# Kernel optimization log

Hardware: AMD Instinct MI355X
Metric: run time of the kernel (lower is better)

The kernel has to match this reference:

```python
import jax, jax.numpy as jnp
import numpy as np

IN_F = 4096
OUT_F = 4096
BLOCK = 8
N_CENTROIDS = 2048
N_BLOCKS = IN_F // BLOCK  # 512
N_TOKENS = 1024


def setup_inputs() -> dict:
    key = jax.random.key(0)
    k1, k2, k3, k4 = jax.random.split(key, 4)
    x = jax.random.normal(k1, (N_TOKENS, IN_F), dtype=jnp.float32)
    centroids = jax.random.normal(k2, (N_CENTROIDS, BLOCK), dtype=jnp.float32)
    # assignments: block-major layout, length n_blocks * out_features
    assignments = jax.random.randint(k3, (N_BLOCKS * OUT_F,), 0, N_CENTROIDS, dtype=jnp.int32)
    bias = jax.random.normal(k4, (OUT_F,), dtype=jnp.float32) * 0.01
    # counts = bincount(assignments), used only in backward (grad averaging)
    counts = jax.ops.segment_sum(
        jnp.ones_like(assignments, dtype=jnp.float32), assignments,
        num_segments=N_CENTROIDS)
    return {"x": x, "centroids": centroids, "bias": bias,
            "assignments": assignments, "counts": counts}


def reference(x, centroids, bias, assignments, counts):
    # weight = centroids[assignments].reshape(n_blocks, out_f, block)
    #                        .permute(1,0,2).reshape(out_f, in_f)
    w = centroids[assignments]  # [n_blocks*out_f, block]
    w = w.reshape(N_BLOCKS, OUT_F, BLOCK).transpose(1, 0, 2).reshape(OUT_F, IN_F)
    # F.linear(x, weight, bias) = x @ w.T + bias
    return x @ w.T + bias
```

## Files before the change

kernel.cpp:

```cpp
#include <hip/hip_runtime.h>
#include <hip/hip_bf16.h>

#define IN_F   4096
#define OUT_F  4096
#define QBLK   8
#define NBLKS  512
#define NTOK   1024
#define NCENT  2048

typedef unsigned int u32;
typedef unsigned short u16;
typedef __attribute__((ext_vector_type(8))) short short8;
typedef __attribute__((ext_vector_type(4))) float floatx4;

__device__ __forceinline__ u16 f2bf(float f) {
  union { float f; u32 u; } v; v.f = f;
  u32 u = v.u;
  return (u16)((u + 0x7fffu + ((u >> 16) & 1u)) >> 16);
}

__device__ __forceinline__ void load_lds_16(const void* g, void* l) {
  __builtin_amdgcn_global_load_lds(
      (const __attribute__((address_space(1))) u32*)g,
      (__attribute__((address_space(3))) u32*)l, 16, 0, 0);
}

__global__ __launch_bounds__(256) void cast_bf16_kernel(
    const float* __restrict__ src, u16* __restrict__ dst) {
  int g = blockIdx.x * 256 + threadIdx.x;
  const float4* sv = (const float4*)src;
  float4 a = sv[(size_t)g * 2];
  float4 b = sv[(size_t)g * 2 + 1];
  union { u16 s[8]; uint4 v; } o;
  o.s[0] = f2bf(a.x); o.s[1] = f2bf(a.y); o.s[2] = f2bf(a.z); o.s[3] = f2bf(a.w);
  o.s[4] = f2bf(b.x); o.s[5] = f2bf(b.y); o.s[6] = f2bf(b.z); o.s[7] = f2bf(b.w);
  ((uint4*)dst)[g] = o.v;
}

__global__ __launch_bounds__(256, 4) void gemm_fused_kernel(
    const u16* __restrict__ A,
    const u16* __restrict__ centb,
    const int* __restrict__ assign,
    const float* __restrict__ bias,
    float* __restrict__ out0,
    float* __restrict__ partials) {
  __shared__ __align__(16) u16 cs[NCENT * 8];
  __shared__ __align__(16) u16 As[128 * 32];

  const int t = threadIdx.x;
  const int lane = t & 63;
  const int wv = t >> 6;
  const int wm = wv >> 1;
  const int wn = wv & 1;
  const int quad = lane >> 4;
  const int r16 = lane & 15;
  const int m0 = blockIdx.y * 128;
  const int n0 = blockIdx.x * 128;
  const int s = blockIdx.z;
  const int kchunk = IN_F / gridDim.z;
  const int k_base = s * kchunk;
  const int iters = kchunk / 32;

#pragma unroll
  for (int it = 0; it < 8; ++it) {
    int c = it * 256 + t;
    load_lds_16(centb + (size_t)c * 8, cs + (size_t)c * 8);
  }

  floatx4 acc[4][4];
#pragma unroll
  for (int i = 0; i < 4; ++i)
#pragma unroll
    for (int j = 0; j < 4; ++j)
#pragma unroll
      for (int r = 0; r < 4; ++r) acc[i][j][r] = 0.0f;

  const int ncol = n0 + wn * 64 + r16;
  const int sq = quad ^ (r16 & 3);

  for (int kt = 0; kt < iters; ++kt) {
    const int k0 = k_base + kt * 32;

    int idxv[4];
    const int kb = (k0 >> 3) + quad;
#pragma unroll
    for (int j = 0; j < 4; ++j)
      idxv[j] = assign[(size_t)kb * OUT_F + ncol + j * 16];

#pragma unroll
    for (int i = 0; i < 2; ++i) {
      int p = i * 256 + t;
      int row = p >> 2;
      int q = (p & 3) ^ (row & 3);
      load_lds_16(A + (size_t)(m0 + row) * IN_F + k0 + q * 8, As + p * 8);
    }
    __syncthreads();

    const short8* Asv = (const short8*)As;
    const short8* csv = (const short8*)cs;
    short8 af[4], bfr[4];
#pragma unroll
    for (int i = 0; i < 4; ++i)
      af[i] = Asv[(wm * 64 + i * 16 + r16) * 4 + sq];
#pragma unroll
    for (int j = 0; j < 4; ++j)
      bfr[j] = csv[idxv[j]];

#pragma unroll
    for (int i = 0; i < 4; ++i)
#pragma unroll
      for (int j = 0; j < 4; ++j)
        acc[i][j] = __builtin_amdgcn_mfma_f32_16x16x32_bf16(af[i], bfr[j], acc[i][j], 0, 0, 0);

    __syncthreads();
  }

  float* C = (s == 0) ? out0 : (partials + (size_t)(s - 1) * NTOK * OUT_F);
  const bool add_bias = (gridDim.z == 1);
  const int row_base = m0 + wm * 64 + quad * 4;
#pragma unroll
  for (int j = 0; j < 4; ++j) {
    const int col = ncol + j * 16;
    const float bv = add_bias ? bias[col] : 0.0f;
#pragma unroll
    for (int i = 0; i < 4; ++i) {
      const int row = row_base + i * 16;
#pragma unroll
      for (int r = 0; r < 4; ++r)
        C[(size_t)(row + r) * OUT_F + col] = acc[i][j][r] + bv;
    }
  }
}

__global__ __launch_bounds__(256) void reduce_kernel(
    float* __restrict__ out, const float* __restrict__ partials,
    const float* __restrict__ bias, int sm1) {
  int g = blockIdx.x * 256 + threadIdx.x;
  float4 v = ((const float4*)out)[g];
  for (int s = 0; s < sm1; ++s) {
    float4 p = ((const float4*)(partials + (size_t)s * NTOK * OUT_F))[g];
    v.x += p.x; v.y += p.y; v.z += p.z; v.w += p.w;
  }
  float4 b = ((const float4*)bias)[g & (OUT_F / 4 - 1)];
  v.x += b.x; v.y += b.y; v.z += b.z; v.w += b.w;
  ((float4*)out)[g] = v;
}

extern "C" void kernel_launch(void* const* d_in, const int* in_sizes, int n_in,
                              void* d_out, int out_size, void* d_ws, size_t ws_size,
                              hipStream_t stream) {
  const float* x      = (const float*)d_in[0];
  const float* cent   = (const float*)d_in[1];
  const float* bias   = (const float*)d_in[2];
  const int*   assign = (const int*)d_in[3];
  float* out = (float*)d_out;

  const size_t xb_bytes   = (size_t)NTOK * IN_F * sizeof(u16);
  const size_t cent_bytes = (size_t)NCENT * 8 * sizeof(u16);
  const size_t part_bytes = (size_t)NTOK * OUT_F * sizeof(float);
  u16*   xb       = (u16*)d_ws;
  u16*   centb    = (u16*)((char*)d_ws + xb_bytes);
  float* partials = (float*)((char*)d_ws + xb_bytes + cent_bytes);

  const size_t base = xb_bytes + cent_bytes;
  int S = 1;
  if (ws_size >= base + 3 * part_bytes) S = 4;
  else if (ws_size >= base + 1 * part_bytes) S = 2;

  hipLaunchKernelGGL(cast_bf16_kernel, dim3((NTOK * IN_F / 8) / 256), dim3(256), 0, stream,
                     x, xb);
  hipLaunchKernelGGL(cast_bf16_kernel, dim3((NCENT * 8 / 8) / 256), dim3(256), 0, stream,
                     cent, centb);
  hipLaunchKernelGGL(gemm_fused_kernel, dim3(OUT_F / 128, NTOK / 128, S), dim3(256), 0, stream,
                     xb, centb, assign, bias, out, partials);
  if (S > 1)
    hipLaunchKernelGGL(reduce_kernel, dim3((NTOK * OUT_F / 4) / 256), dim3(256), 0, stream,
                       out, partials, bias, S - 1);
}
```

Baseline: 131.2 us.

## Pre-swizzle activations into fragment layout and register-prefetch A directly from global

The cast kernel now writes x in bf16 in a layout grouped by 16 rows and 8-element k-blocks, so each MFMA lane can load its A fragment straight from global memory with one 16-byte load. The A tile in LDS and both per-iteration barriers are removed, and the A fragments and assignment indices for the next k-step are prefetched into registers. MFMA issue priority is raised with setprio, and launch bounds drop to 3 waves per SIMD to make room for the extra registers. In exchange, A is no longer shared through LDS across the two N-waves of a block, so global and L2 traffic for activations roughly doubles.

```diff
diff --git a/kernel.cpp b/kernel.cpp
--- a/kernel.cpp
+++ b/kernel.cpp
@@ -37,15 +37,40 @@
   ((uint4*)dst)[g] = o.v;
 }
 
-__global__ __launch_bounds__(256, 4) void gemm_fused_kernel(
-    const u16* __restrict__ A,
+__global__ __launch_bounds__(256) void cast_swz_kernel(
+    const float* __restrict__ src, u16* __restrict__ dst) {
+  __shared__ __align__(16) u16 ls[256 * 8];
+  const int b = blockIdx.x;
+  const int mg = b >> 5;
+  const int kq = b & 31;
+  const int t = threadIdx.x;
+  const int ml = t >> 4;
+  const int kbl = t & 15;
+
+  const float* p = src + (size_t)(mg * 16 + ml) * IN_F + kq * 128 + kbl * 8;
+  float4 a = ((const float4*)p)[0];
+  float4 c = ((const float4*)p)[1];
+  union { u16 s[8]; uint4 v; } o;
+  o.s[0] = f2bf(a.x); o.s[1] = f2bf(a.y); o.s[2] = f2bf(a.z); o.s[3] = f2bf(a.w);
+  o.s[4] = f2bf(c.x); o.s[5] = f2bf(c.y); o.s[6] = f2bf(c.z); o.s[7] = f2bf(c.w);
+
+  const int cidx = (kbl << 4) | (ml ^ kbl);
+  *(uint4*)&ls[cidx * 8] = o.v;
+  __syncthreads();
+
+  const int g = (t & 0xF0) | ((t & 15) ^ ((t >> 4) & 15));
+  uint4* dbase = (uint4*)(dst + (size_t)(mg * 512 + kq * 16) * 128);
+  dbase[g] = ((const uint4*)ls)[t];
+}
+
+__global__ __launch_bounds__(256, 3) void gemm_fused_kernel(
+    const u16* __restrict__ xs,
     const u16* __restrict__ centb,
     const int* __restrict__ assign,
     const float* __restrict__ bias,
     float* __restrict__ out0,
     float* __restrict__ partials) {
   __shared__ __align__(16) u16 cs[NCENT * 8];
-  __shared__ __align__(16) u16 As[128 * 32];
 
   const int t = threadIdx.x;
   const int lane = t & 63;
@@ -58,7 +83,7 @@
   const int n0 = blockIdx.x * 128;
   const int s = blockIdx.z;
   const int kchunk = IN_F / gridDim.z;
-  const int k_base = s * kchunk;
+  const int kb0 = (s * kchunk) >> 3;
   const int iters = kchunk / 32;
 
 #pragma unroll
@@ -76,43 +101,52 @@
       for (int r = 0; r < 4; ++r) acc[i][j][r] = 0.0f;
 
   const int ncol = n0 + wn * 64 + r16;
-  const int sq = quad ^ (r16 & 3);
+  const short8* xv = (const short8*)xs;
+  const short8* csv = (const short8*)cs;
+
+  const int mgrp0 = (m0 >> 4) + wm * 4;
+  size_t abase[4];
+#pragma unroll
+  for (int i = 0; i < 4; ++i)
+    abase[i] = ((size_t)(mgrp0 + i) * 512 + kb0 + quad) * 16 + r16;
+
+  const int* aptr = assign + (size_t)(kb0 + quad) * OUT_F + ncol;
+
+  short8 afc[4];
+#pragma unroll
+  for (int i = 0; i < 4; ++i) afc[i] = xv[abase[i]];
+  int idxc[4];
+#pragma unroll
+  for (int j = 0; j < 4; ++j) idxc[j] = aptr[j * 16];
+
+  __syncthreads();
 
   for (int kt = 0; kt < iters; ++kt) {
-    const int k0 = k_base + kt * 32;
-
-    int idxv[4];
-    const int kb = (k0 >> 3) + quad;
-#pragma unroll
-    for (int j = 0; j < 4; ++j)
-      idxv[j] = assign[(size_t)kb * OUT_F + ncol + j * 16];
-
-#pragma unroll
-    for (int i = 0; i < 2; ++i) {
-      int p = i * 256 + t;
-      int row = p >> 2;
-      int q = (p & 3) ^ (row & 3);
-      load_lds_16(A + (size_t)(m0 + row) * IN_F + k0 + q * 8, As + p * 8);
+    short8 afn[4];
+    int idxn[4];
+    if (kt + 1 < iters) {
+#pragma unroll
+      for (int i = 0; i < 4; ++i) afn[i] = xv[abase[i] + (size_t)(kt + 1) * 64];
+#pragma unroll
+      for (int j = 0; j < 4; ++j) idxn[j] = aptr[(size_t)(kt + 1) * 4 * OUT_F + j * 16];
     }
-    __syncthreads();
-
-    const short8* Asv = (const short8*)As;
-    const short8* csv = (const short8*)cs;
-    short8 af[4], bfr[4];
+
+    short8 bfr[4];
+#pragma unroll
+    for (int j = 0; j < 4; ++j) bfr[j] = csv[idxc[j]];
+
+    __builtin_amdgcn_s_setprio(1);
 #pragma unroll
     for (int i = 0; i < 4; ++i)
-      af[i] = Asv[(wm * 64 + i * 16 + r16) * 4 + sq];
-#pragma unroll
-    for (int j = 0; j < 4; ++j)
-      bfr[j] = csv[idxv[j]];
-
-#pragma unroll
-    for (int i = 0; i < 4; ++i)
 #pragma unroll
       for (int j = 0; j < 4; ++j)
-        acc[i][j] = __builtin_amdgcn_mfma_f32_16x16x32_bf16(af[i], bfr[j], acc[i][j], 0, 0, 0);
-
-    __syncthreads();
+        acc[i][j] = __builtin_amdgcn_mfma_f32_16x16x32_bf16(afc[i], bfr[j], acc[i][j], 0, 0, 0);
+    __builtin_amdgcn_s_setprio(0);
+
+#pragma unroll
+    for (int i = 0; i < 4; ++i) afc[i] = afn[i];
+#pragma unroll
+    for (int j = 0; j < 4; ++j) idxc[j] = idxn[j];
   }
 
   float* C = (s == 0) ? out0 : (partials + (size_t)(s - 1) * NTOK * OUT_F);
@@ -158,7 +192,7 @@
   const size_t xb_bytes   = (size_t)NTOK * IN_F * sizeof(u16);
   const size_t cent_bytes = (size_t)NCENT * 8 * sizeof(u16);
   const size_t part_bytes = (size_t)NTOK * OUT_F * sizeof(float);
-  u16*   xb       = (u16*)d_ws;
+  u16*   xs       = (u16*)d_ws;
   u16*   centb    = (u16*)((char*)d_ws + xb_bytes);
   float* partials = (float*)((char*)d_ws + xb_bytes + cent_bytes);
 
@@ -167,12 +201,11 @@
   if (ws_size >= base + 3 * part_bytes) S = 4;
   else if (ws_size >= base + 1 * part_bytes) S = 2;
 
-  hipLaunchKernelGGL(cast_bf16_kernel, dim3((NTOK * IN_F / 8) / 256), dim3(256), 0, stream,
-                     x, xb);
+  hipLaunchKernelGGL(cast_swz_kernel, dim3(64 * 32), dim3(256), 0, stream, x, xs);
   hipLaunchKernelGGL(cast_bf16_kernel, dim3((NCENT * 8 / 8) / 256), dim3(256), 0, stream,
                      cent, centb);
   hipLaunchKernelGGL(gemm_fused_kernel, dim3(OUT_F / 128, NTOK / 128, S), dim3(256), 0, stream,
-                     xb, centb, assign, bias, out, partials);
+                     xs, centb, assign, bias, out, partials);
   if (S > 1)
     hipLaunchKernelGGL(reduce_kernel, dim3((NTOK * OUT_F / 4) / 256), dim3(256), 0, stream,
                        out, partials, bias, S - 1);
```

Result: slower. 136.7 us (+4.2%).

## Double-buffer A tile in LDS and prefetch next assignment indices

Applied to the files above, without the earlier changes.

Adds a second LDS buffer for the A tile and issues the next tile's global-to-LDS loads and next assignment-index loads before computing the current tile. The two per-iteration __syncthreads are replaced by one explicit vmcnt wait plus barrier, so global-load latency overlaps MFMA work. Split-K is now fixed at compile time to 4 and always uses the reduce kernel, no longer checking workspace size. That risks out-of-bounds writes if the workspace cannot hold three partial buffers, and the extra LDS buffer may lower occupancy.

```diff
diff --git a/kernel.cpp b/kernel.cpp
--- a/kernel.cpp
+++ b/kernel.cpp
@@ -7,6 +7,10 @@
 #define NBLKS  512
 #define NTOK   1024
 #define NCENT  2048
+
+#define SPLITK 4
+#define KCHUNK (IN_F / SPLITK)
+#define KITERS (KCHUNK / 32)
 
 typedef unsigned int u32;
 typedef unsigned short u16;
@@ -45,7 +49,7 @@
     float* __restrict__ out0,
     float* __restrict__ partials) {
   __shared__ __align__(16) u16 cs[NCENT * 8];
-  __shared__ __align__(16) u16 As[128 * 32];
+  __shared__ __align__(16) u16 As[2][128 * 32];
 
   const int t = threadIdx.x;
   const int lane = t & 63;
@@ -57,9 +61,8 @@
   const int m0 = blockIdx.y * 128;
   const int n0 = blockIdx.x * 128;
   const int s = blockIdx.z;
-  const int kchunk = IN_F / gridDim.z;
-  const int k_base = s * kchunk;
-  const int iters = kchunk / 32;
+  const int kb0 = (s * KCHUNK) >> 3;
+  const int k_base = kb0 << 3;
 
 #pragma unroll
   for (int it = 0; it < 8; ++it) {
@@ -67,6 +70,17 @@
     load_lds_16(centb + (size_t)c * 8, cs + (size_t)c * 8);
   }
 
+  {
+    const int p0 = t;
+#pragma unroll
+    for (int i = 0; i < 2; ++i) {
+      int p = i * 256 + p0;
+      int row = p >> 2;
+      int q = (p & 3) ^ (row & 3);
+      load_lds_16(A + (size_t)(m0 + row) * IN_F + k_base + q * 8, &As[0][p * 8]);
+    }
+  }
+
   floatx4 acc[4][4];
 #pragma unroll
   for (int i = 0; i < 4; ++i)
@@ -77,34 +91,42 @@
 
   const int ncol = n0 + wn * 64 + r16;
   const int sq = quad ^ (r16 & 3);
-
-  for (int kt = 0; kt < iters; ++kt) {
-    const int k0 = k_base + kt * 32;
-
-    int idxv[4];
-    const int kb = (k0 >> 3) + quad;
-#pragma unroll
-    for (int j = 0; j < 4; ++j)
-      idxv[j] = assign[(size_t)kb * OUT_F + ncol + j * 16];
-
-#pragma unroll
-    for (int i = 0; i < 2; ++i) {
-      int p = i * 256 + t;
-      int row = p >> 2;
-      int q = (p & 3) ^ (row & 3);
-      load_lds_16(A + (size_t)(m0 + row) * IN_F + k0 + q * 8, As + p * 8);
-    }
-    __syncthreads();
-
-    const short8* Asv = (const short8*)As;
-    const short8* csv = (const short8*)cs;
+  const int* ai = assign + (size_t)kb0 * OUT_F;
+  const u32 vi = (u32)(quad * OUT_F + ncol);
+
+  int idxc[4], idxn[4];
+#pragma unroll
+  for (int j = 0; j < 4; ++j) idxc[j] = ai[vi + (u32)(j * 16)];
+  __syncthreads();
+
+  const short8* csv = (const short8*)cs;
+  int buf = 0;
+
+  for (int kt = 0; kt < KITERS; ++kt) {
+    const bool not_last = (kt + 1 < KITERS);
+    if (not_last) {
+      const int k0n = k_base + (kt + 1) * 32;
+#pragma unroll
+      for (int i = 0; i < 2; ++i) {
+        int p = i * 256 + t;
+        int row = p >> 2;
+        int q = (p & 3) ^ (row & 3);
+        load_lds_16(A + (size_t)(m0 + row) * IN_F + k0n + q * 8,
+                    &As[buf ^ 1][p * 8]);
+      }
+      __builtin_amdgcn_sched_barrier(0);
+      const int* an = ai + (size_t)(kt + 1) * 4 * OUT_F;
+#pragma unroll
+      for (int j = 0; j < 4; ++j) idxn[j] = an[vi + (u32)(j * 16)];
+    }
+
+    const short8* Asv = (const short8*)As[buf];
     short8 af[4], bfr[4];
 #pragma unroll
     for (int i = 0; i < 4; ++i)
       af[i] = Asv[(wm * 64 + i * 16 + r16) * 4 + sq];
 #pragma unroll
-    for (int j = 0; j < 4; ++j)
-      bfr[j] = csv[idxv[j]];
+    for (int j = 0; j < 4; ++j) bfr[j] = csv[idxc[j]];
 
 #pragma unroll
     for (int i = 0; i < 4; ++i)
@@ -112,16 +134,25 @@
       for (int j = 0; j < 4; ++j)
         acc[i][j] = __builtin_amdgcn_mfma_f32_16x16x32_bf16(af[i], bfr[j], acc[i][j], 0, 0, 0);
 
-    __syncthreads();
+#pragma unroll
+    for (int j = 0; j < 4; ++j) idxc[j] = idxn[j];
+
+    if (not_last) {
+      __builtin_amdgcn_sched_barrier(0);
+      asm volatile("s_waitcnt vmcnt(4)" ::: "memory");
+      __builtin_amdgcn_sched_barrier(0);
+      __builtin_amdgcn_s_barrier();
+      __builtin_amdgcn_sched_barrier(0);
+    }
+    buf ^= 1;
   }
 
   float* C = (s == 0) ? out0 : (partials + (size_t)(s - 1) * NTOK * OUT_F);
-  const bool add_bias = (gridDim.z == 1);
   const int row_base = m0 + wm * 64 + quad * 4;
 #pragma unroll
   for (int j = 0; j < 4; ++j) {
     const int col = ncol + j * 16;
-    const float bv = add_bias ? bias[col] : 0.0f;
+    const float bv = 0.0f;
 #pragma unroll
     for (int i = 0; i < 4; ++i) {
       const int row = row_base + i * 16;
@@ -157,23 +188,16 @@
 
   const size_t xb_bytes   = (size_t)NTOK * IN_F * sizeof(u16);
   const size_t cent_bytes = (size_t)NCENT * 8 * sizeof(u16);
-  const size_t part_bytes = (size_t)NTOK * OUT_F * sizeof(float);
   u16*   xb       = (u16*)d_ws;
   u16*   centb    = (u16*)((char*)d_ws + xb_bytes);
   float* partials = (float*)((char*)d_ws + xb_bytes + cent_bytes);
-
-  const size_t base = xb_bytes + cent_bytes;
-  int S = 1;
-  if (ws_size >= base + 3 * part_bytes) S = 4;
-  else if (ws_size >= base + 1 * part_bytes) S = 2;
 
   hipLaunchKernelGGL(cast_bf16_kernel, dim3((NTOK * IN_F / 8) / 256), dim3(256), 0, stream,
                      x, xb);
   hipLaunchKernelGGL(cast_bf16_kernel, dim3((NCENT * 8 / 8) / 256), dim3(256), 0, stream,
                      cent, centb);
-  hipLaunchKernelGGL(gemm_fused_kernel, dim3(OUT_F / 128, NTOK / 128, S), dim3(256), 0, stream,
+  hipLaunchKernelGGL(gemm_fused_kernel, dim3(OUT_F / 128, NTOK / 128, SPLITK), dim3(256), 0, stream,
                      xb, centb, assign, bias, out, partials);
-  if (S > 1)
-    hipLaunchKernelGGL(reduce_kernel, dim3((NTOK * OUT_F / 4) / 256), dim3(256), 0, stream,
-                       out, partials, bias, S - 1);
-}
+  hipLaunchKernelGGL(reduce_kernel, dim3((NTOK * OUT_F / 4) / 256), dim3(256), 0, stream,
+                     out, partials, bias, SPLITK - 1);
+}
```

After: 157.2 us. 1.2x slower.
